# Kernel optimization log

Measured on AMD Instinct MI355X. Metric: run time of the kernel, lower is better.

The kernel has to match this reference:

```python
import jax, jax.numpy as jnp
import numpy as np

EPS = 1e-8  # torch F.cosine_similarity norm clamp
TEMPERATURE = 0.05


def setup_inputs() -> dict:
    key = jax.random.key(0)
    k1, k2 = jax.random.split(key)
    N, D = 8192, 768
    query_embeddings = jax.random.normal(k1, (N, D), dtype=jnp.float32)
    content_embeddings = jax.random.normal(k2, (N, D), dtype=jnp.float32)
    return {"query_embeddings": query_embeddings, "content_embeddings": content_embeddings}


def reference(query_embeddings, content_embeddings):
    # cosine_similarity(q[:,None], c[None,:], dim=2) == normalize(q) @ normalize(c).T
    qn = query_embeddings / jnp.maximum(
        jnp.linalg.norm(query_embeddings, axis=-1, keepdims=True), EPS)
    cn = content_embeddings / jnp.maximum(
        jnp.linalg.norm(content_embeddings, axis=-1, keepdims=True), EPS)
    sim = jnp.einsum('nd,md->nm', qn, cn) / TEMPERATURE  # [N, N]
    # cross-entropy with targets = arange(N): positive is the diagonal
    logz = jax.nn.logsumexp(sim, axis=-1)                # [N]
    loss = jnp.mean(logz - jnp.diagonal(sim))
    return loss
```

## Files before the change

kernel.cpp:

```cpp
#include <hip/hip_runtime.h>
#include <hip/hip_bf16.h>


#define NROWS 8192
#define DDIM  768
#define ROWB  1536
#define NKT  (DDIM / 64)
#define NIT  (NKT / 2)
#define GRID_T (NROWS / 256)

constexpr float INV_TEMP = 20.0f;
constexpr float NORM_EPS = 1e-8f;

using bf16 = __hip_bfloat16;
typedef __attribute__((ext_vector_type(4))) float  f32x4;
typedef __attribute__((ext_vector_type(8))) short  bf16x8;

__global__ void norm_diag_kernel(const float* __restrict__ q, const float* __restrict__ c,
                                 bf16* __restrict__ qn, bf16* __restrict__ cn,
                                 float* __restrict__ diag) {
    const int row  = (blockIdx.x * 256 + threadIdx.x) >> 6;
    const int lane = threadIdx.x & 63;
    const float4* qv = (const float4*)(q + (size_t)row * DDIM);
    const float4* cv = (const float4*)(c + (size_t)row * DDIM);
    float4 a[3], b[3];
    #pragma unroll
    for (int j = 0; j < 3; ++j) { a[j] = qv[lane + j * 64]; b[j] = cv[lane + j * 64]; }
    float ssq = 0.f, ssc = 0.f, dot = 0.f;
    #pragma unroll
    for (int j = 0; j < 3; ++j) {
        ssq += a[j].x * a[j].x + a[j].y * a[j].y + a[j].z * a[j].z + a[j].w * a[j].w;
        ssc += b[j].x * b[j].x + b[j].y * b[j].y + b[j].z * b[j].z + b[j].w * b[j].w;
        dot += a[j].x * b[j].x + a[j].y * b[j].y + a[j].z * b[j].z + a[j].w * b[j].w;
    }
    #pragma unroll
    for (int m = 32; m; m >>= 1) {
        ssq += __shfl_xor(ssq, m);
        ssc += __shfl_xor(ssc, m);
        dot += __shfl_xor(dot, m);
    }
    float invq = 1.0f / fmaxf(sqrtf(ssq), NORM_EPS);
    float invc = 1.0f / fmaxf(sqrtf(ssc), NORM_EPS);
    if (lane == 0) diag[row] = dot * invq * invc * INV_TEMP;
    ushort4* qo = (ushort4*)(qn + (size_t)row * DDIM);
    ushort4* co = (ushort4*)(cn + (size_t)row * DDIM);
    #pragma unroll
    for (int j = 0; j < 3; ++j) {
        union { ushort4 u; bf16 h[4]; } oq, oc;
        oq.h[0] = __float2bfloat16(a[j].x * invq); oq.h[1] = __float2bfloat16(a[j].y * invq);
        oq.h[2] = __float2bfloat16(a[j].z * invq); oq.h[3] = __float2bfloat16(a[j].w * invq);
        oc.h[0] = __float2bfloat16(b[j].x * invc); oc.h[1] = __float2bfloat16(b[j].y * invc);
        oc.h[2] = __float2bfloat16(b[j].z * invc); oc.h[3] = __float2bfloat16(b[j].w * invc);
        qo[lane + j * 64] = oq.u;
        co[lane + j * 64] = oc.u;
    }
}

__device__ __forceinline__ void async16(void* l, const void* g) {
    __builtin_amdgcn_global_load_lds(
        (const __attribute__((address_space(1))) void*)g,
        (__attribute__((address_space(3))) void*)l, 16, 0, 0);
}

#define BARRIER __builtin_amdgcn_s_barrier()
#define SCHED0  __builtin_amdgcn_sched_barrier(0)
#define PRIO1   __builtin_amdgcn_s_setprio(1)
#define PRIO0   __builtin_amdgcn_s_setprio(0)
#define VMCNT(n) do { asm volatile("s_waitcnt vmcnt(" #n ")" ::: "memory"); } while (0)

#define STAGE_A(P, H, KT) do {                                              \
    const char* _g = aG + (size_t)(H) * 128 * ROWB + (size_t)(KT) * 128;    \
    char* _l = lds + (P) * 65536 + (H) * 16384 + dstW;                      \
    async16(_l, _g);                                                        \
    async16(_l + 8192, _g + 64 * ROWB);                                     \
} while (0)
#define STAGE_B(P, H, KT) do {                                              \
    const char* _g = bG + (size_t)(H) * 128 * ROWB + (size_t)(KT) * 128;    \
    char* _l = lds + 32768 + (P) * 65536 + (H) * 16384 + dstW;              \
    async16(_l, _g);                                                        \
    async16(_l + 8192, _g + 64 * ROWB);                                     \
} while (0)

#define READ_A(P, MH) do {                                                  \
    const char* _ab = lds + (P) * 65536 + aBaseT + (MH) * 64 * 128;         \
    _Pragma("unroll") for (int mi = 0; mi < 4; ++mi) {                      \
        a[mi][0] = *(const bf16x8*)(_ab + mi * 2048 + xk0);                 \
        a[mi][1] = *(const bf16x8*)(_ab + mi * 2048 + xk1);                 \
    }                                                                       \
} while (0)
#define READ_B(P, NH) do {                                                  \
    const char* _bb = lds + 32768 + (P) * 65536 + bBaseT + (NH) * 32 * 128; \
    _Pragma("unroll") for (int ni = 0; ni < 2; ++ni) {                      \
        bfr[NH][ni][0] = *(const bf16x8*)(_bb + ni * 2048 + xk0);           \
        bfr[NH][ni][1] = *(const bf16x8*)(_bb + ni * 2048 + xk1);           \
    }                                                                       \
} while (0)

#define MFMA_Q(MH, NH)                                                      \
    _Pragma("unroll") for (int mi = 0; mi < 4; ++mi)                        \
    _Pragma("unroll") for (int ni = 0; ni < 2; ++ni) {                      \
        acc[(MH)*4+mi][(NH)*2+ni] = __builtin_amdgcn_mfma_f32_16x16x32_bf16(\
            a[mi][0], bfr[NH][ni][0], acc[(MH)*4+mi][(NH)*2+ni], 0, 0, 0);  \
        acc[(MH)*4+mi][(NH)*2+ni] = __builtin_amdgcn_mfma_f32_16x16x32_bf16(\
            a[mi][1], bfr[NH][ni][1], acc[(MH)*4+mi][(NH)*2+ni], 0, 0, 0);  \
    }

__launch_bounds__(512, 2)
__global__ void simgemm_kernel(const bf16* __restrict__ A, const bf16* __restrict__ B,
                               float* __restrict__ partial) {
    __shared__ __attribute__((aligned(16))) char smem[131072];
    char* lds = smem;

    const int bid = blockIdx.x;
    const int tm = bid >> 5, tn = bid & 31;
    const int rowBase = tm * 256, colBase = tn * 256;
    const int tid = threadIdx.x;
    const int wid = tid >> 6, lane = tid & 63;
    const int wr = wid >> 2, wc = wid & 3;

    const int sr  = tid >> 3;
    const int scb = ((tid & 7) * 16) ^ ((sr & 7) << 4);
    const char* aG = (const char*)A + (size_t)(rowBase + sr) * ROWB + scb;
    const char* bG = (const char*)B + (size_t)(colBase + sr) * ROWB + scb;
    const int dstW = wid * 1024;

    const int aBaseT = wr * 16384 + (lane & 15) * 128;
    const int bBaseT = (wc >> 1) * 16384 + ((wc & 1) * 64 + (lane & 15)) * 128;
    const int klane  = (lane >> 4) * 16;
    const int swzr   = (lane & 7) << 4;
    const int xk0    = klane ^ swzr;
    const int xk1    = (64 + klane) ^ swzr;

    f32x4  acc[8][4] = {};
    bf16x8 a[4][2];
    bf16x8 bfr[2][2][2];

    STAGE_A(0, 0, 0); STAGE_A(0, 1, 0);
    STAGE_B(0, 0, 0); STAGE_B(0, 1, 0);
    STAGE_A(1, 0, 1); STAGE_A(1, 1, 1);
    VMCNT(4);
    BARRIER; SCHED0;
    READ_A(0, 0); READ_B(0, 0);
    SCHED0;

    #pragma unroll 1
    for (int i = 0; i < NIT; ++i) {
        const int t1 = 2 * i + 1;
        const int t2 = 2 * i + 2, t3 = 2 * i + 3;
        const bool more = (i + 1 < NIT);
        STAGE_B(1, 0, t1);
        PRIO1; MFMA_Q(0, 0); PRIO0;
        VMCNT(6);
        BARRIER; SCHED0;
        READ_B(0, 1); SCHED0;
        STAGE_B(1, 1, t1);
        PRIO1; MFMA_Q(0, 1); PRIO0;
        BARRIER; SCHED0;
        READ_A(0, 1); SCHED0;
        if (more) STAGE_A(0, 0, t2);
        PRIO1; MFMA_Q(1, 0); PRIO0;
        BARRIER; SCHED0;
        if (more) STAGE_A(0, 1, t2);
        PRIO1; MFMA_Q(1, 1); PRIO0;
        if (more) { VMCNT(6); } else { VMCNT(0); }
        BARRIER; SCHED0;
        READ_A(1, 0); READ_B(1, 0); SCHED0;
        if (more) STAGE_B(0, 0, t2);
        PRIO1; MFMA_Q(0, 0); PRIO0;
        if (more) { VMCNT(6); }
        BARRIER; SCHED0;
        READ_B(1, 1); SCHED0;
        if (more) STAGE_B(0, 1, t2);
        PRIO1; MFMA_Q(0, 1); PRIO0;
        BARRIER; SCHED0;
        READ_A(1, 1); SCHED0;
        if (more) STAGE_A(1, 0, t3);
        PRIO1; MFMA_Q(1, 0); PRIO0;
        BARRIER; SCHED0;
        if (more) STAGE_A(1, 1, t3);
        PRIO1; MFMA_Q(1, 1); PRIO0;
        if (more) { VMCNT(6); }
        BARRIER; SCHED0;
        if (more) { READ_A(0, 0); READ_B(0, 0); SCHED0; }
    }

    __syncthreads();
    float* red = (float*)smem;
    #pragma unroll
    for (int m = 0; m < 8; ++m) {
        #pragma unroll
        for (int r = 0; r < 4; ++r) {
            float s = 0.f;
            #pragma unroll
            for (int n = 0; n < 4; ++n)
                s += __expf(fmaf(INV_TEMP, acc[m][n][r], -INV_TEMP));
            s += __shfl_xor(s, 1);
            s += __shfl_xor(s, 2);
            s += __shfl_xor(s, 4);
            s += __shfl_xor(s, 8);
            if ((lane & 15) == 0)
                red[(wr * 128 + m * 16 + (lane >> 4) * 4 + r) * 4 + wc] = s;
        }
    }
    __syncthreads();
    if (tid < 256)
        partial[(size_t)(rowBase + tid) * GRID_T + tn] =
            red[tid * 4 + 0] + red[tid * 4 + 1] + red[tid * 4 + 2] + red[tid * 4 + 3];
}

__global__ void finalize_kernel(const float* __restrict__ partial,
                                const float* __restrict__ diag,
                                float* __restrict__ out) {
    int row = blockIdx.x * 256 + threadIdx.x;
    const float4* p = (const float4*)(partial + (size_t)row * GRID_T);
    float z = 0.f;
    #pragma unroll
    for (int i = 0; i < GRID_T / 4; ++i) {
        float4 v = p[i];
        z += v.x + v.y + v.z + v.w;
    }
    float term = INV_TEMP + logf(z) - diag[row];
    #pragma unroll
    for (int m = 32; m; m >>= 1) term += __shfl_xor(term, m);
    __shared__ float wsum[4];
    if ((threadIdx.x & 63) == 0) wsum[threadIdx.x >> 6] = term;
    __syncthreads();
    if (threadIdx.x == 0) {
        float s = wsum[0] + wsum[1] + wsum[2] + wsum[3];
        atomicAdd(out, s * (1.0f / NROWS));
    }
}

extern "C" void kernel_launch(void* const* d_in, const int* in_sizes, int n_in,
                              void* d_out, int out_size, void* d_ws, size_t ws_size,
                              hipStream_t stream) {
    const float* q = (const float*)d_in[0];
    const float* c = (const float*)d_in[1];
    float* out = (float*)d_out;

    char* ws = (char*)d_ws;
    bf16* qn = (bf16*)ws;
    bf16* cn = (bf16*)(ws + (size_t)NROWS * DDIM * 2);
    float* diag = (float*)(ws + (size_t)NROWS * DDIM * 4);
    float* partial = diag + NROWS;

    hipMemsetAsync(d_out, 0, sizeof(float), stream);

    norm_diag_kernel<<<NROWS / 4, 256, 0, stream>>>(q, c, qn, cn, diag);
    simgemm_kernel<<<GRID_T * GRID_T, 512, 0, stream>>>(qn, cn, partial);
    finalize_kernel<<<NROWS / 256, 256, 0, stream>>>(partial, diag, out);
}
```

Baseline: 191.2 us.

## Make GEMM blocks persistent over four column tiles with continuous K pipeline

Each workgroup now handles one row panel against four consecutive 256-column tiles, so the grid drops from 1024 blocks to 256. The global-to-LDS prefetch pipeline runs through all tile boundaries without draining. At each tile end the exp-sum epilogue runs in a separate LDS region, then the accumulators are reset. The aim is to remove per-block prologue and epilogue drain and to overlap the epilogue with loads already in flight for the next tile. The cost is a smaller grid that may fill the CUs less evenly, extra barriers at tile transitions, and slightly more LDS.

```diff
diff --git a/kernel.cpp b/kernel.cpp
--- a/kernel.cpp
+++ b/kernel.cpp
@@ -5,9 +5,10 @@
 #define NROWS 8192
 #define DDIM  768
 #define ROWB  1536
-#define NKT  (DDIM / 64)
-#define NIT  (NKT / 2)
+#define PANEL (256 * ROWB)
 #define GRID_T (NROWS / 256)
+#define NTILE 4
+#define NITT  24
 
 constexpr float INV_TEMP = 20.0f;
 constexpr float NORM_EPS = 1e-8f;
@@ -67,15 +68,16 @@
 #define PRIO1   __builtin_amdgcn_s_setprio(1)
 #define PRIO0   __builtin_amdgcn_s_setprio(0)
 #define VMCNT(n) do { asm volatile("s_waitcnt vmcnt(" #n ")" ::: "memory"); } while (0)
-
-#define STAGE_A(P, H, KT) do {                                              \
-    const char* _g = aG + (size_t)(H) * 128 * ROWB + (size_t)(KT) * 128;    \
+#define LGKM0   do { asm volatile("s_waitcnt lgkmcnt(0)" ::: "memory"); SCHED0; } while (0)
+
+#define STAGE_A(P, H, K) do {                                               \
+    const char* _g = aG + (size_t)(H) * 128 * ROWB + (size_t)(K) * 128;     \
     char* _l = lds + (P) * 65536 + (H) * 16384 + dstW;                      \
     async16(_l, _g);                                                        \
     async16(_l + 8192, _g + 64 * ROWB);                                     \
 } while (0)
-#define STAGE_B(P, H, KT) do {                                              \
-    const char* _g = bG + (size_t)(H) * 128 * ROWB + (size_t)(KT) * 128;    \
+#define STAGE_B(P, H, BP, K) do {                                           \
+    const char* _g = (BP) + (size_t)(H) * 128 * ROWB + (size_t)(K) * 128;   \
     char* _l = lds + 32768 + (P) * 65536 + (H) * 16384 + dstW;              \
     async16(_l, _g);                                                        \
     async16(_l + 8192, _g + 64 * ROWB);                                     \
@@ -108,12 +110,13 @@
 __launch_bounds__(512, 2)
 __global__ void simgemm_kernel(const bf16* __restrict__ A, const bf16* __restrict__ B,
                                float* __restrict__ partial) {
-    __shared__ __attribute__((aligned(16))) char smem[131072];
+    __shared__ __attribute__((aligned(16))) char smem[131072 + 4096];
     char* lds = smem;
 
     const int bid = blockIdx.x;
-    const int tm = bid >> 5, tn = bid & 31;
-    const int rowBase = tm * 256, colBase = tn * 256;
+    const int tm = bid >> 3;
+    int tn = (bid & 7) * 4;
+    const int rowBase = tm * 256;
     const int tid = threadIdx.x;
     const int wid = tid >> 6, lane = tid & 63;
     const int wr = wid >> 2, wc = wid & 3;
@@ -121,7 +124,7 @@
     const int sr  = tid >> 3;
     const int scb = ((tid & 7) * 16) ^ ((sr & 7) << 4);
     const char* aG = (const char*)A + (size_t)(rowBase + sr) * ROWB + scb;
-    const char* bG = (const char*)B + (size_t)(colBase + sr) * ROWB + scb;
+    const char* bG = (const char*)B + (size_t)(tn * 256 + sr) * ROWB + scb;
     const int dstW = wid * 1024;
 
     const int aBaseT = wr * 16384 + (lane & 15) * 128;
@@ -135,77 +138,94 @@
     bf16x8 a[4][2];
     bf16x8 bfr[2][2][2];
 
+    int k1 = 1, k2 = 2, k3 = 3;
+    const char *b1 = bG, *b2 = bG, *b3 = bG;
+    int ec = 0;
+
     STAGE_A(0, 0, 0); STAGE_A(0, 1, 0);
-    STAGE_B(0, 0, 0); STAGE_B(0, 1, 0);
+    STAGE_B(0, 0, bG, 0); STAGE_B(0, 1, bG, 0);
     STAGE_A(1, 0, 1); STAGE_A(1, 1, 1);
     VMCNT(4);
     BARRIER; SCHED0;
-    READ_A(0, 0); READ_B(0, 0);
+    READ_B(0, 0); READ_A(0, 0);
     SCHED0;
 
     #pragma unroll 1
-    for (int i = 0; i < NIT; ++i) {
-        const int t1 = 2 * i + 1;
-        const int t2 = 2 * i + 2, t3 = 2 * i + 3;
-        const bool more = (i + 1 < NIT);
-        STAGE_B(1, 0, t1);
+    for (int ii = 0; ii < NITT; ++ii) {
+        const bool more = (ii + 1 < NITT);
+        STAGE_B(1, 0, b1, k1);
         PRIO1; MFMA_Q(0, 0); PRIO0;
         VMCNT(6);
         BARRIER; SCHED0;
         READ_B(0, 1); SCHED0;
-        STAGE_B(1, 1, t1);
+        STAGE_B(1, 1, b1, k1);
         PRIO1; MFMA_Q(0, 1); PRIO0;
         BARRIER; SCHED0;
         READ_A(0, 1); SCHED0;
-        if (more) STAGE_A(0, 0, t2);
+        if (more) STAGE_A(0, 0, k2);
         PRIO1; MFMA_Q(1, 0); PRIO0;
         BARRIER; SCHED0;
-        if (more) STAGE_A(0, 1, t2);
+        if (more) STAGE_A(0, 1, k2);
         PRIO1; MFMA_Q(1, 1); PRIO0;
         if (more) { VMCNT(6); } else { VMCNT(0); }
         BARRIER; SCHED0;
-        READ_A(1, 0); READ_B(1, 0); SCHED0;
-        if (more) STAGE_B(0, 0, t2);
+        READ_B(1, 0); READ_A(1, 0); SCHED0;
+        if (more) STAGE_B(0, 0, b2, k2);
         PRIO1; MFMA_Q(0, 0); PRIO0;
         if (more) { VMCNT(6); }
         BARRIER; SCHED0;
         READ_B(1, 1); SCHED0;
-        if (more) STAGE_B(0, 1, t2);
+        if (more) STAGE_B(0, 1, b2, k2);
         PRIO1; MFMA_Q(0, 1); PRIO0;
         BARRIER; SCHED0;
         READ_A(1, 1); SCHED0;
-        if (more) STAGE_A(1, 0, t3);
+        if (more) STAGE_A(1, 0, k3);
         PRIO1; MFMA_Q(1, 0); PRIO0;
         BARRIER; SCHED0;
-        if (more) STAGE_A(1, 1, t3);
+        if (more) STAGE_A(1, 1, k3);
         PRIO1; MFMA_Q(1, 1); PRIO0;
         if (more) { VMCNT(6); }
         BARRIER; SCHED0;
-        if (more) { READ_A(0, 0); READ_B(0, 0); SCHED0; }
-    }
-
-    __syncthreads();
-    float* red = (float*)smem;
-    #pragma unroll
-    for (int m = 0; m < 8; ++m) {
-        #pragma unroll
-        for (int r = 0; r < 4; ++r) {
-            float s = 0.f;
+        if (more) { READ_B(0, 0); READ_A(0, 0); SCHED0; }
+
+        k1 += 2; if (k1 >= 12) { k1 -= 12; b1 += PANEL; }
+        k2 += 2; if (k2 >= 12) { k2 -= 12; b2 += PANEL; }
+        k3 += 2; if (k3 >= 12) { k3 -= 12; b3 += PANEL; }
+
+        if (++ec == 6) {
+            ec = 0;
+            float* red = (float*)(lds + 131072);
             #pragma unroll
-            for (int n = 0; n < 4; ++n)
-                s += __expf(fmaf(INV_TEMP, acc[m][n][r], -INV_TEMP));
-            s += __shfl_xor(s, 1);
-            s += __shfl_xor(s, 2);
-            s += __shfl_xor(s, 4);
-            s += __shfl_xor(s, 8);
-            if ((lane & 15) == 0)
-                red[(wr * 128 + m * 16 + (lane >> 4) * 4 + r) * 4 + wc] = s;
+            for (int m = 0; m < 8; ++m) {
+                #pragma unroll
+                for (int r = 0; r < 4; ++r) {
+                    float s = 0.f;
+                    #pragma unroll
+                    for (int n = 0; n < 4; ++n)
+                        s += __expf(fmaf(INV_TEMP, acc[m][n][r], -INV_TEMP));
+                    s += __shfl_xor(s, 1);
+                    s += __shfl_xor(s, 2);
+                    s += __shfl_xor(s, 4);
+                    s += __shfl_xor(s, 8);
+                    if ((lane & 15) == 0)
+                        red[(wr * 128 + m * 16 + (lane >> 4) * 4 + r) * 4 + wc] = s;
+                }
+            }
+            LGKM0;
+            BARRIER; SCHED0;
+            if (tid < 256)
+                partial[(size_t)(rowBase + tid) * GRID_T + tn] =
+                    red[tid * 4 + 0] + red[tid * 4 + 1] +
+                    red[tid * 4 + 2] + red[tid * 4 + 3];
+            ++tn;
+            #pragma unroll
+            for (int m = 0; m < 8; ++m)
+                #pragma unroll
+                for (int n = 0; n < 4; ++n)
+                    acc[m][n] = (f32x4){0.f, 0.f, 0.f, 0.f};
+            BARRIER; SCHED0;
         }
     }
-    __syncthreads();
-    if (tid < 256)
-        partial[(size_t)(rowBase + tid) * GRID_T + tn] =
-            red[tid * 4 + 0] + red[tid * 4 + 1] + red[tid * 4 + 2] + red[tid * 4 + 3];
 }
 
 __global__ void finalize_kernel(const float* __restrict__ partial,
@@ -247,6 +267,6 @@
     hipMemsetAsync(d_out, 0, sizeof(float), stream);
 
     norm_diag_kernel<<<NROWS / 4, 256, 0, stream>>>(q, c, qn, cn, diag);
-    simgemm_kernel<<<GRID_T * GRID_T, 512, 0, stream>>>(qn, cn, partial);
+    simgemm_kernel<<<256, 512, 0, stream>>>(qn, cn, partial);
     finalize_kernel<<<NROWS / 256, 256, 0, stream>>>(partial, diag, out);
 }
```

Measured after the change: 200.3 us. +4.7%, slower.

## Switch similarity GEMM to 32x32x16 bf16 MFMA tiles

Applied to the files above, without the earlier changes.

Replaces the 16x16x32 MFMA instruction with the 32x32x16 variant, restructuring the per-wave fragments, LDS read addressing (four k-slices per 128-byte row) and accumulator layout (f32x16). The epilogue's exp-sum reduction is remapped to the 32x32 output lane layout, adding a shuffle step. The goal is fewer MFMA issues and LDS reads per FLOP for higher matrix-core throughput, at the cost of different register pressure and a new LDS bank-access pattern under the existing swizzle.

```diff
diff --git a/kernel.cpp b/kernel.cpp
--- a/kernel.cpp
+++ b/kernel.cpp
@@ -13,8 +13,8 @@
 constexpr float NORM_EPS = 1e-8f;
 
 using bf16 = __hip_bfloat16;
-typedef __attribute__((ext_vector_type(4))) float  f32x4;
-typedef __attribute__((ext_vector_type(8))) short  bf16x8;
+typedef __attribute__((ext_vector_type(16))) float f32x16;
+typedef __attribute__((ext_vector_type(8)))  short bf16x8;
 
 __global__ void norm_diag_kernel(const float* __restrict__ q, const float* __restrict__ c,
                                  bf16* __restrict__ qn, bf16* __restrict__ cn,
@@ -82,28 +82,22 @@
 } while (0)
 
 #define READ_A(P, MH) do {                                                  \
-    const char* _ab = lds + (P) * 65536 + aBaseT + (MH) * 64 * 128;         \
-    _Pragma("unroll") for (int mi = 0; mi < 4; ++mi) {                      \
-        a[mi][0] = *(const bf16x8*)(_ab + mi * 2048 + xk0);                 \
-        a[mi][1] = *(const bf16x8*)(_ab + mi * 2048 + xk1);                 \
-    }                                                                       \
+    const char* _ab = lds + (P) * 65536 + aBaseT + (MH) * 8192;             \
+    _Pragma("unroll") for (int mi = 0; mi < 2; ++mi)                        \
+    _Pragma("unroll") for (int ks = 0; ks < 4; ++ks)                        \
+        a[mi][ks] = *(const bf16x8*)(_ab + mi * 4096 + xkk[ks]);            \
 } while (0)
 #define READ_B(P, NH) do {                                                  \
-    const char* _bb = lds + 32768 + (P) * 65536 + bBaseT + (NH) * 32 * 128; \
-    _Pragma("unroll") for (int ni = 0; ni < 2; ++ni) {                      \
-        bfr[NH][ni][0] = *(const bf16x8*)(_bb + ni * 2048 + xk0);           \
-        bfr[NH][ni][1] = *(const bf16x8*)(_bb + ni * 2048 + xk1);           \
-    }                                                                       \
+    const char* _bb = lds + 32768 + (P) * 65536 + bBaseT + (NH) * 4096;     \
+    _Pragma("unroll") for (int ks = 0; ks < 4; ++ks)                        \
+        bfr[NH][ks] = *(const bf16x8*)(_bb + xkk[ks]);                      \
 } while (0)
 
 #define MFMA_Q(MH, NH)                                                      \
-    _Pragma("unroll") for (int mi = 0; mi < 4; ++mi)                        \
-    _Pragma("unroll") for (int ni = 0; ni < 2; ++ni) {                      \
-        acc[(MH)*4+mi][(NH)*2+ni] = __builtin_amdgcn_mfma_f32_16x16x32_bf16(\
-            a[mi][0], bfr[NH][ni][0], acc[(MH)*4+mi][(NH)*2+ni], 0, 0, 0);  \
-        acc[(MH)*4+mi][(NH)*2+ni] = __builtin_amdgcn_mfma_f32_16x16x32_bf16(\
-            a[mi][1], bfr[NH][ni][1], acc[(MH)*4+mi][(NH)*2+ni], 0, 0, 0);  \
-    }
+    _Pragma("unroll") for (int mi = 0; mi < 2; ++mi)                        \
+    _Pragma("unroll") for (int ks = 0; ks < 4; ++ks)                        \
+        acc[(MH)*2+mi][NH] = __builtin_amdgcn_mfma_f32_32x32x16_bf16(       \
+            a[mi][ks], bfr[NH][ks], acc[(MH)*2+mi][NH], 0, 0, 0);
 
 __launch_bounds__(512, 2)
 __global__ void simgemm_kernel(const bf16* __restrict__ A, const bf16* __restrict__ B,
@@ -124,23 +118,24 @@
     const char* bG = (const char*)B + (size_t)(colBase + sr) * ROWB + scb;
     const int dstW = wid * 1024;
 
-    const int aBaseT = wr * 16384 + (lane & 15) * 128;
-    const int bBaseT = (wc >> 1) * 16384 + ((wc & 1) * 64 + (lane & 15)) * 128;
-    const int klane  = (lane >> 4) * 16;
-    const int swzr   = (lane & 7) << 4;
-    const int xk0    = klane ^ swzr;
-    const int xk1    = (64 + klane) ^ swzr;
-
-    f32x4  acc[8][4] = {};
-    bf16x8 a[4][2];
-    bf16x8 bfr[2][2][2];
+    const int aBaseT = wr * 16384 + (lane & 31) * 128;
+    const int bBaseT = (wc >> 1) * 16384 + (wc & 1) * 8192 + (lane & 31) * 128;
+    const int kl2  = (lane >> 5) * 16;
+    const int swzr = (lane & 7) << 4;
+    int xkk[4];
+    #pragma unroll
+    for (int ks = 0; ks < 4; ++ks) xkk[ks] = (ks * 32 + kl2) ^ swzr;
+
+    f32x16 acc[4][2] = {};
+    bf16x8 a[2][4];
+    bf16x8 bfr[2][4];
 
     STAGE_A(0, 0, 0); STAGE_A(0, 1, 0);
     STAGE_B(0, 0, 0); STAGE_B(0, 1, 0);
     STAGE_A(1, 0, 1); STAGE_A(1, 1, 1);
     VMCNT(4);
     BARRIER; SCHED0;
-    READ_A(0, 0); READ_B(0, 0);
+    READ_B(0, 0); READ_A(0, 0);
     SCHED0;
 
     #pragma unroll 1
@@ -164,7 +159,7 @@
         PRIO1; MFMA_Q(1, 1); PRIO0;
         if (more) { VMCNT(6); } else { VMCNT(0); }
         BARRIER; SCHED0;
-        READ_A(1, 0); READ_B(1, 0); SCHED0;
+        READ_B(1, 0); READ_A(1, 0); SCHED0;
         if (more) STAGE_B(0, 0, t2);
         PRIO1; MFMA_Q(0, 0); PRIO0;
         if (more) { VMCNT(6); }
@@ -181,25 +176,24 @@
         PRIO1; MFMA_Q(1, 1); PRIO0;
         if (more) { VMCNT(6); }
         BARRIER; SCHED0;
-        if (more) { READ_A(0, 0); READ_B(0, 0); SCHED0; }
+        if (more) { READ_B(0, 0); READ_A(0, 0); SCHED0; }
     }
 
     __syncthreads();
     float* red = (float*)smem;
     #pragma unroll
-    for (int m = 0; m < 8; ++m) {
+    for (int F = 0; F < 4; ++F) {
         #pragma unroll
-        for (int r = 0; r < 4; ++r) {
-            float s = 0.f;
-            #pragma unroll
-            for (int n = 0; n < 4; ++n)
-                s += __expf(fmaf(INV_TEMP, acc[m][n][r], -INV_TEMP));
+        for (int r = 0; r < 16; ++r) {
+            float s = __expf(fmaf(INV_TEMP, acc[F][0][r], -INV_TEMP))
+                    + __expf(fmaf(INV_TEMP, acc[F][1][r], -INV_TEMP));
             s += __shfl_xor(s, 1);
             s += __shfl_xor(s, 2);
             s += __shfl_xor(s, 4);
             s += __shfl_xor(s, 8);
-            if ((lane & 15) == 0)
-                red[(wr * 128 + m * 16 + (lane >> 4) * 4 + r) * 4 + wc] = s;
+            s += __shfl_xor(s, 16);
+            if ((lane & 31) == 0)
+                red[(wr * 128 + F * 32 + (r & 3) + 8 * (r >> 2) + 4 * (lane >> 5)) * 4 + wc] = s;
         }
     }
     __syncthreads();
```

Measured after the change: 226.9 us. 18.7% more time.

## Coarsen GEMM pipeline to two MFMA quadrants per barrier phase

Applied to the files above, without the earlier changes.

Restructures the main loop of the similarity GEMM so each barrier phase issues two MFMA quadrants back-to-back, with paired global-to-LDS stages and adjusted vmcnt waits. This halves the number of workgroup barriers per iteration and gives longer uninterrupted MFMA runs. In exchange, loads are issued in larger bursts and there is less fine-grained overlap between LDS reads, global staging and compute. The changed wait counts also risk hazards on the LDS buffers if they are miscounted.

```diff
diff --git a/kernel.cpp b/kernel.cpp
--- a/kernel.cpp
+++ b/kernel.cpp
@@ -140,7 +140,7 @@
     STAGE_A(1, 0, 1); STAGE_A(1, 1, 1);
     VMCNT(4);
     BARRIER; SCHED0;
-    READ_A(0, 0); READ_B(0, 0);
+    READ_B(0, 0); READ_A(0, 0);
     SCHED0;
 
     #pragma unroll 1
@@ -148,40 +148,26 @@
         const int t1 = 2 * i + 1;
         const int t2 = 2 * i + 2, t3 = 2 * i + 3;
         const bool more = (i + 1 < NIT);
-        STAGE_B(1, 0, t1);
-        PRIO1; MFMA_Q(0, 0); PRIO0;
-        VMCNT(6);
-        BARRIER; SCHED0;
+        STAGE_B(1, 0, t1); STAGE_B(1, 1, t1);
         READ_B(0, 1); SCHED0;
-        STAGE_B(1, 1, t1);
-        PRIO1; MFMA_Q(0, 1); PRIO0;
+        PRIO1; MFMA_Q(0, 0); MFMA_Q(0, 1); PRIO0;
         BARRIER; SCHED0;
         READ_A(0, 1); SCHED0;
-        if (more) STAGE_A(0, 0, t2);
-        PRIO1; MFMA_Q(1, 0); PRIO0;
-        BARRIER; SCHED0;
-        if (more) STAGE_A(0, 1, t2);
-        PRIO1; MFMA_Q(1, 1); PRIO0;
-        if (more) { VMCNT(6); } else { VMCNT(0); }
-        BARRIER; SCHED0;
-        READ_A(1, 0); READ_B(1, 0); SCHED0;
-        if (more) STAGE_B(0, 0, t2);
-        PRIO1; MFMA_Q(0, 0); PRIO0;
-        if (more) { VMCNT(6); }
-        BARRIER; SCHED0;
+        if (more) { STAGE_A(0, 0, t2); STAGE_A(0, 1, t2); }
+        PRIO1; MFMA_Q(1, 0); MFMA_Q(1, 1); PRIO0;
+        if (more) { VMCNT(4); } else { VMCNT(0); }
+        BARRIER; SCHED0;
+        READ_B(1, 0); READ_A(1, 0); SCHED0;
+        if (more) { STAGE_B(0, 0, t2); STAGE_B(0, 1, t2); }
         READ_B(1, 1); SCHED0;
-        if (more) STAGE_B(0, 1, t2);
-        PRIO1; MFMA_Q(0, 1); PRIO0;
+        PRIO1; MFMA_Q(0, 0); MFMA_Q(0, 1); PRIO0;
         BARRIER; SCHED0;
         READ_A(1, 1); SCHED0;
-        if (more) STAGE_A(1, 0, t3);
-        PRIO1; MFMA_Q(1, 0); PRIO0;
-        BARRIER; SCHED0;
-        if (more) STAGE_A(1, 1, t3);
-        PRIO1; MFMA_Q(1, 1); PRIO0;
-        if (more) { VMCNT(6); }
-        BARRIER; SCHED0;
-        if (more) { READ_A(0, 0); READ_B(0, 0); SCHED0; }
+        if (more) { STAGE_A(1, 0, t3); STAGE_A(1, 1, t3); }
+        PRIO1; MFMA_Q(1, 0); MFMA_Q(1, 1); PRIO0;
+        if (more) { VMCNT(4); }
+        BARRIER; SCHED0;
+        if (more) { READ_B(0, 0); READ_A(0, 0); SCHED0; }
     }
 
     __syncthreads();
```

New measurement: 192.2 us. About the same (+0.5%).
